# Kernel optimization log

Hardware: AMD Instinct MI355X
Metric: run time of the kernel (lower is better)

## Reference

```python
import jax, jax.numpy as jnp
import numpy as np

N_NODES = 15000
N_EDGES = 40000
N_GRAPHS = 750
D = 64
NODE_DIM = 32
EDGE_DIM = 16
NUM_CONV = 3
S2S_STEPS = 3


def setup_inputs() -> dict:
    key = jax.random.key(0)
    ks = jax.random.split(key, 24)
    s = 0.05
    inp = {
        'x': jax.random.normal(ks[0], (N_NODES, NODE_DIM), jnp.float32),
        'edge_attr': jax.random.uniform(ks[1], (N_EDGES, EDGE_DIM), jnp.float32),
        'edge_index': jax.random.randint(ks[2], (2, N_EDGES), 0, N_NODES),
        'batch': jnp.sort(jax.random.randint(ks[3], (N_NODES,), 0, N_GRAPHS)),
        # input projection
        'in_W': jax.random.normal(ks[4], (NODE_DIM, D)) * s,
        'in_b': jnp.zeros((D,)),
        # edge MLP -> per-edge DxD weights
        'e1_W': jax.random.normal(ks[5], (EDGE_DIM, D)) * s,
        'e1_b': jnp.zeros((D,)),
        'e2_W': jax.random.normal(ks[6], (D, D * D)) * s,
        'e2_b': jnp.zeros((D * D,)),
        'conv_b': jnp.zeros((D,)),
        # GRU (gate order r,z,n like torch)
        'gru_Wih': jax.random.normal(ks[7], (3 * D, D)) * s,
        'gru_Whh': jax.random.normal(ks[8], (3 * D, D)) * s,
        'gru_bih': jnp.zeros((3 * D,)),
        'gru_bhh': jnp.zeros((3 * D,)),
        # Set2Set LSTM (gate order i,f,g,o like torch), input 2D -> hidden D
        'lstm_Wih': jax.random.normal(ks[9], (4 * D, 2 * D)) * s,
        'lstm_Whh': jax.random.normal(ks[10], (4 * D, D)) * s,
        'lstm_bih': jnp.zeros((4 * D,)),
        'lstm_bhh': jnp.zeros((4 * D,)),
        # output MLP
        'out1_W': jax.random.normal(ks[11], (2 * D, 2 * D)) * s,
        'out1_b': jnp.zeros((2 * D,)),
        'out2_W': jax.random.normal(ks[12], (2 * D, 1)) * s,
        'out2_b': jnp.zeros((1,)),
    }
    return inp


def _gru_cell(m, h, Wih, Whh, bih, bhh):
    gi = m @ Wih.T + bih
    gh = h @ Whh.T + bhh
    ir, iz, inn = jnp.split(gi, 3, axis=-1)
    hr, hz, hn = jnp.split(gh, 3, axis=-1)
    r = jax.nn.sigmoid(ir + hr)
    z = jax.nn.sigmoid(iz + hz)
    n = jnp.tanh(inn + r * hn)
    return (1.0 - z) * n + z * h


def _lstm_cell(q, h, c, Wih, Whh, bih, bhh):
    g = q @ Wih.T + bih + h @ Whh.T + bhh
    i, f, gg, o = jnp.split(g, 4, axis=-1)
    c = jax.nn.sigmoid(f) * c + jax.nn.sigmoid(i) * jnp.tanh(gg)
    h = jax.nn.sigmoid(o) * jnp.tanh(c)
    return h, c


def reference(x, edge_attr, edge_index, batch,
              in_W, in_b, e1_W, e1_b, e2_W, e2_b, conv_b,
              gru_Wih, gru_Whh, gru_bih, gru_bhh,
              lstm_Wih, lstm_Whh, lstm_bih, lstm_bhh,
              out1_W, out1_b, out2_W, out2_b):
    src, dst = edge_index[0], edge_index[1]
    out = jax.nn.relu(x @ in_W + in_b)           # [N, D]
    h = out
    # edge-conditioned weights (edge_attr is constant across conv iters)
    W_e = (jax.nn.relu(edge_attr @ e1_W + e1_b) @ e2_W + e2_b).reshape(-1, D, D)  # [E, D, D]
    deg = jnp.maximum(jax.ops.segment_sum(jnp.ones((N_EDGES,), out.dtype), dst, N_NODES), 1.0)
    for _ in range(NUM_CONV):
        msg = jnp.einsum('ed,edf->ef', out[src], W_e)          # per-edge matmul
        agg = jax.ops.segment_sum(msg, dst, N_NODES) / deg[:, None]  # scatter-mean
        m = jax.nn.relu(agg + conv_b)
        h = _gru_cell(m, h, gru_Wih, gru_Whh, gru_bih, gru_bhh)
        out = h
    # Set2Set pooling
    q_star = jnp.zeros((N_GRAPHS, 2 * D), out.dtype)
    hl = jnp.zeros((N_GRAPHS, D), out.dtype)
    cl = jnp.zeros((N_GRAPHS, D), out.dtype)
    for _ in range(S2S_STEPS):
        hl, cl = _lstm_cell(q_star, hl, cl, lstm_Wih, lstm_Whh, lstm_bih, lstm_bhh)
        q = hl
        e = jnp.sum(out * q[batch], axis=-1)                    # [N]
        e = e - jax.ops.segment_max(e, batch, N_GRAPHS)[batch]
        ee = jnp.exp(e)
        a = ee / jax.ops.segment_sum(ee, batch, N_GRAPHS)[batch]
        r = jax.ops.segment_sum(a[:, None] * out, batch, N_GRAPHS)  # [G, D]
        q_star = jnp.concatenate([q, r], axis=-1)
    z = jax.nn.relu(q_star @ out1_W + out1_b) @ out2_W + out2_b
    return z
```

## Files before the change

### kernel.cpp

```cpp
#include <hip/hip_runtime.h>
#include <math.h>

#define N_NODES 15000
#define N_EDGES 40000
#define N_GRAPHS 750
#define N_TILES 938
#define N_TILES_PAD 944

typedef __attribute__((ext_vector_type(8))) short bf16x8;
typedef __attribute__((ext_vector_type(4))) float f32x4;

__device__ __forceinline__ float sigmoidf_(float x) { return 1.f / (1.f + expf(-x)); }

__device__ __forceinline__ unsigned short f2bf(float v) {
    unsigned u = __float_as_uint(v);
    unsigned r = (u + 0x7FFFu + ((u >> 16) & 1u)) >> 16;
    return (unsigned short)r;
}
__device__ __forceinline__ float bf2f(unsigned short b) {
    return __uint_as_float(((unsigned)b) << 16);
}


__global__ void tscan_kernel(const int* __restrict__ tcnt, int* __restrict__ tptr,
                             int* __restrict__ cursor) {
    __shared__ int buf[1024];
    int t = threadIdx.x;
    int v = (t < N_TILES) ? tcnt[t] : 0;
    buf[t] = v;
    __syncthreads();
    for (int ofs = 1; ofs < 1024; ofs <<= 1) {
        int a = (t >= ofs) ? buf[t - ofs] : 0;
        __syncthreads();
        buf[t] += a;
        __syncthreads();
    }
    int excl = buf[t] - v;
    if (t <= N_TILES_PAD) tptr[t] = excl;
    if (t < N_TILES) cursor[t] = excl;
}

__global__ void fillpack_kernel(const int* __restrict__ src, int* __restrict__ cursor,
                                int* __restrict__ edge_list,
                                const float* __restrict__ node_h,
                                unsigned short* __restrict__ Apack) {
    int b = blockIdx.x;
    int tid = threadIdx.x;
    if (b < 157) {
        int e = b * 256 + tid;
        if (e < N_EDGES) {
            int slot = atomicAdd(&cursor[src[e] >> 4], 1);
            edge_list[slot] = e;
        }
    } else {
        int nt = b - 157;
        for (int idx = tid; idx < 1024; idx += 256) {
            int kt = idx >> 9, lane = (idx >> 3) & 63, j = idx & 7;
            int quad = lane >> 4, m = lane & 15;
            int n = nt * 16 + m;
            float v = (n < N_NODES) ? node_h[(size_t)n * 64 + kt * 32 + quad * 8 + j] : 0.f;
            unsigned short hi = f2bf(v);
            Apack[nt * 2048 + kt * 1024 + lane * 8 + j] = hi;
            Apack[nt * 2048 + kt * 1024 + 512 + lane * 8 + j] = f2bf(v - bf2f(hi));
        }
    }
}

__global__ __launch_bounds__(256)
void prep_kernel(const float* __restrict__ x, const float* __restrict__ in_W,
                 const float* __restrict__ in_b, float* __restrict__ node_h,
                 const float* __restrict__ e2b,
                 const float* __restrict__ ea, const float* __restrict__ e1_W,
                 const float* __restrict__ e1_b, float* __restrict__ h1,
                 const float* __restrict__ e2W,
                 unsigned short* __restrict__ Bhi, unsigned short* __restrict__ Blo,
                 const float* __restrict__ lWih, const float* __restrict__ lWhh,
                 const float* __restrict__ gWih, const float* __restrict__ gWhh,
                 float* __restrict__ lWihT, float* __restrict__ lWhhT,
                 unsigned short* __restrict__ gWihP, unsigned short* __restrict__ gWhhP,
                 const int* __restrict__ batch, int* __restrict__ gptr,
                 const int* __restrict__ src, const int* __restrict__ dst,
                 int* __restrict__ tcnt, float* __restrict__ deg) {
    int b = blockIdx.x;
    int tid = threadIdx.x;
    if (b < 938) {
        __shared__ float xs[4][32];
        int n0 = b * 16;
        for (int g2 = 0; g2 < 4; ++g2) {
            int nb = n0 + g2 * 4;
            __syncthreads();
            if (tid < 128) {
                int xi = nb * 32 + tid;
                xs[tid >> 5][tid & 31] = (xi < N_NODES * 32) ? x[xi] : 0.f;
            }
            __syncthreads();
            int nn = tid >> 6, f = tid & 63;
            float s = in_b[f];
            #pragma unroll
            for (int i = 0; i < 32; ++i) s += xs[nn][i] * in_W[i * 64 + f];
            if (nb + nn < N_NODES) node_h[(size_t)(nb + nn) * 64 + f] = fmaxf(s, 0.f);
        }
    } else if (b < 2188) {
        __shared__ float eas[4][16];
        int e0 = (b - 938) * 32;
        for (int g2 = 0; g2 < 8; ++g2) {
            int eb = e0 + g2 * 4;
            __syncthreads();
            if (tid < 64) eas[tid >> 4][tid & 15] = ea[eb * 16 + tid];
            __syncthreads();
            int nn = tid >> 6, f = tid & 63;
            float s = e1_b[f];
            #pragma unroll
            for (int i = 0; i < 16; ++i) s += eas[nn][i] * e1_W[i * 64 + f];
            h1[(size_t)(eb + nn) * 64 + f] = fmaxf(s, 0.f);
        }
    } else if (b < 3244) {
        int idx = (b - 2188) * 256 + tid;
        int j = idx & 7, lane = (idx >> 3) & 63, kt = (idx >> 9) & 1;
        int rem = idx >> 10;
        int ct = rem % 33, ft = rem / 33;
        int d = kt * 32 + ((lane >> 4) << 3) + j;
        int m = lane & 15;
        float v;
        if (ct < 32) {
            int c = ct * 16 + m;
            int kk = c >> 3, fi = c & 7;
            v = e2W[(size_t)kk * 4096 + d * 64 + ft * 8 + fi];
        } else {
            v = (m < 8) ? e2b[d * 64 + ft * 8 + m] : 0.f;
        }
        unsigned short hi = f2bf(v);
        Bhi[idx] = hi;
        Blo[idx] = f2bf(v - bf2f(hi));
    } else if (b < 3436) {
        int idx = (b - 3244) * 256 + tid;
        if (idx < 32768) {
            int i = idx >> 8, r = idx & 255;
            lWihT[i * 256 + r] = lWih[r * 128 + i];
        } else if (idx < 49152) {
            int x2 = idx - 32768; int i = x2 >> 8, r = x2 & 255;
            lWhhT[i * 256 + r] = lWhh[r * 64 + i];
        }
    } else if (b < 3532) {
        int idx = (b - 3436) * 256 + tid;
        if (idx < 12288) {
            int j = idx & 7, lane = (idx >> 3) & 63, kt = (idx >> 9) & 1, ct = idx >> 10;
            int k = kt * 32 + ((lane >> 4) << 3) + j;
            int n = ct * 16 + (lane & 15);
            float v = gWih[n * 64 + k];
            unsigned short hi = f2bf(v);
            gWihP[idx] = hi;
            gWihP[12288 + idx] = f2bf(v - bf2f(hi));
        } else {
            int i2 = idx - 12288;
            int j = i2 & 7, lane = (i2 >> 3) & 63, kt = (i2 >> 9) & 1, ct = i2 >> 10;
            int k = kt * 32 + ((lane >> 4) << 3) + j;
            int n = ct * 16 + (lane & 15);
            float v = gWhh[n * 64 + k];
            unsigned short hi = f2bf(v);
            gWhhP[i2] = hi;
            gWhhP[12288 + i2] = f2bf(v - bf2f(hi));
        }
    } else if (b < 3591) {
        int n = (b - 3532) * 256 + tid;
        if (n < N_NODES) {
            int bb = batch[n];
            int pb = (n == 0) ? -1 : batch[n - 1];
            for (int g = pb + 1; g <= bb; ++g) gptr[g] = n;
            if (n == N_NODES - 1)
                for (int g = bb + 1; g <= N_GRAPHS; ++g) gptr[g] = N_NODES;
        }
    } else {
        int e = (b - 3591) * 256 + tid;
        if (e < N_EDGES) {
            atomicAdd(&tcnt[src[e] >> 4], 1);
            atomicAdd(&deg[dst[e]], 1.f);
        }
    }
}

__global__ __launch_bounds__(256, 4)
void conv_kernel(const unsigned short* __restrict__ Apack, const float* __restrict__ h1,
                 const unsigned short* __restrict__ Bhi, const unsigned short* __restrict__ Blo,
                 const int* __restrict__ tptr, const int* __restrict__ edge_list,
                 const int* __restrict__ src, const int* __restrict__ dst,
                 float* __restrict__ agg) {
    __shared__ float T_lds[16 * 548];
    int bid = blockIdx.x;
    int nt = bid % N_TILES_PAD, ft = bid / N_TILES_PAD;
    int n0 = nt * 16;
    int tid = threadIdx.x;
    int lane = tid & 63, wave = tid >> 6;
    int quad = lane >> 4, m = lane & 15;

    int te0 = tptr[nt], te1 = tptr[nt + 1];
    int fi = tid & 7, slot = tid >> 3;
    int cA = te0 + slot, cB = cA + 32;
    int eA = (cA < te1) ? edge_list[cA] : -1;
    int eB = (cB < te1) ? edge_list[cB] : -1;
    int sA_ = 0, dA_ = 0, sB_ = 0, dB_ = 0;
    float4 pa0 = make_float4(0.f, 0.f, 0.f, 0.f), pa1 = pa0, pb0 = pa0, pb1 = pa0;
    if (eA >= 0) {
        sA_ = src[eA]; dA_ = dst[eA];
        pa0 = *(const float4*)(h1 + (size_t)eA * 64);
        pa1 = *(const float4*)(h1 + (size_t)eA * 64 + 4);
    }
    if (eB >= 0) {
        sB_ = src[eB]; dB_ = dst[eB];
        pb0 = *(const float4*)(h1 + (size_t)eB * 64);
        pb1 = *(const float4*)(h1 + (size_t)eB * 64 + 4);
    }

    const unsigned short* ap = Apack + nt * 2048 + lane * 8;
    bf16x8 ahi[2], alo[2];
    ahi[0] = *(const bf16x8*)(ap);
    alo[0] = *(const bf16x8*)(ap + 512);
    ahi[1] = *(const bf16x8*)(ap + 1024);
    alo[1] = *(const bf16x8*)(ap + 1536);

    size_t base0 = (size_t)(ft * 33 + wave) * 1024 + lane * 8;
    const unsigned short* ph = Bhi + base0;
    const unsigned short* pl = Blo + base0;
    bf16x8 bh0 = *(const bf16x8*)(ph);
    bf16x8 bh1 = *(const bf16x8*)(ph + 512);
    bf16x8 bl0 = *(const bf16x8*)(pl);
    bf16x8 bl1 = *(const bf16x8*)(pl + 512);

    int nct = (wave == 0) ? 9 : 8;
    #pragma unroll 1
    for (int ci = 0; ci < nct; ++ci) {
        bf16x8 ch0 = bh0, ch1 = bh1, cl0 = bl0, cl1 = bl1;
        if (ci + 1 < nct) {
            const unsigned short* nh = ph + (size_t)(ci + 1) * 4096;
            const unsigned short* nl = pl + (size_t)(ci + 1) * 4096;
            bh0 = *(const bf16x8*)(nh);
            bh1 = *(const bf16x8*)(nh + 512);
            bl0 = *(const bf16x8*)(nl);
            bl1 = *(const bf16x8*)(nl + 512);
        }
        f32x4 accA = {0.f, 0.f, 0.f, 0.f};
        f32x4 accB = {0.f, 0.f, 0.f, 0.f};
        accA = __builtin_amdgcn_mfma_f32_16x16x32_bf16(ahi[0], ch0, accA, 0, 0, 0);
        accB = __builtin_amdgcn_mfma_f32_16x16x32_bf16(ahi[1], ch1, accB, 0, 0, 0);
        accA = __builtin_amdgcn_mfma_f32_16x16x32_bf16(alo[0], ch0, accA, 0, 0, 0);
        accB = __builtin_amdgcn_mfma_f32_16x16x32_bf16(alo[1], ch1, accB, 0, 0, 0);
        accA = __builtin_amdgcn_mfma_f32_16x16x32_bf16(ahi[0], cl0, accA, 0, 0, 0);
        accB = __builtin_amdgcn_mfma_f32_16x16x32_bf16(ahi[1], cl1, accB, 0, 0, 0);
        int ct = wave + ci * 4;
        int c = ct * 16 + m;
        int kk = c >> 3, fo = c & 7;
        #pragma unroll
        for (int r = 0; r < 4; ++r)
            T_lds[(quad * 4 + r) * 548 + fo * 68 + kk] = accA[r] + accB[r];
    }
    __syncthreads();

    if (eA >= 0) {
        int nn0 = sA_ - n0;
        int nn1 = (eB >= 0 ? sB_ : sA_) - n0;
        const float* h0p = h1 + (size_t)eA * 64;
        const float* h1p = h1 + (size_t)(eB >= 0 ? eB : eA) * 64;
        const float* T0 = &T_lds[nn0 * 548 + fi * 68];
        const float* T1 = &T_lds[nn1 * 548 + fi * 68];
        float p00 = T0[64], p01 = 0.f, p10 = T1[64], p11 = 0.f;
        {
            float4 ta = *(const float4*)(T0);
            float4 tb = *(const float4*)(T0 + 4);
            float4 tc = *(const float4*)(T1);
            float4 td = *(const float4*)(T1 + 4);
            p00 += pa0.x * ta.x + pa0.y * ta.y + pa0.z * ta.z + pa0.w * ta.w;
            p01 += pa1.x * tb.x + pa1.y * tb.y + pa1.z * tb.z + pa1.w * tb.w;
            p10 += pb0.x * tc.x + pb0.y * tc.y + pb0.z * tc.z + pb0.w * tc.w;
            p11 += pb1.x * td.x + pb1.y * td.y + pb1.z * td.z + pb1.w * td.w;
        }
        #pragma unroll
        for (int k4 = 8; k4 < 64; k4 += 8) {
            float4 ha = *(const float4*)(h0p + k4);
            float4 ta = *(const float4*)(T0 + k4);
            float4 hb = *(const float4*)(h0p + k4 + 4);
            float4 tb = *(const float4*)(T0 + k4 + 4);
            float4 hc = *(const float4*)(h1p + k4);
            float4 tc = *(const float4*)(T1 + k4);
            float4 hd = *(const float4*)(h1p + k4 + 4);
            float4 td = *(const float4*)(T1 + k4 + 4);
            p00 += ha.x * ta.x + ha.y * ta.y + ha.z * ta.z + ha.w * ta.w;
            p01 += hb.x * tb.x + hb.y * tb.y + hb.z * tb.z + hb.w * tb.w;
            p10 += hc.x * tc.x + hc.y * tc.y + hc.z * tc.z + hc.w * tc.w;
            p11 += hd.x * td.x + hd.y * td.y + hd.z * td.z + hd.w * td.w;
        }
        atomicAdd(&agg[(size_t)dA_ * 64 + ft * 8 + fi], p00 + p01);
        if (eB >= 0) atomicAdd(&agg[(size_t)dB_ * 64 + ft * 8 + fi], p10 + p11);
    }
    for (int c = cA + 64; c < te1; c += 64) {
        int c1 = c + 32;
        bool h2 = (c1 < te1);
        int e0 = edge_list[c];
        int e1 = h2 ? edge_list[c1] : e0;
        int nn0 = src[e0] - n0, nn1 = src[e1] - n0;
        const float* h0p = h1 + (size_t)e0 * 64;
        const float* h1p = h1 + (size_t)e1 * 64;
        const float* T0 = &T_lds[nn0 * 548 + fi * 68];
        const float* T1 = &T_lds[nn1 * 548 + fi * 68];
        float p00 = T0[64], p01 = 0.f, p10 = T1[64], p11 = 0.f;
        #pragma unroll
        for (int k4 = 0; k4 < 64; k4 += 8) {
            float4 ha = *(const float4*)(h0p + k4);
            float4 ta = *(const float4*)(T0 + k4);
            float4 hb = *(const float4*)(h0p + k4 + 4);
            float4 tb = *(const float4*)(T0 + k4 + 4);
            float4 hc = *(const float4*)(h1p + k4);
            float4 tc = *(const float4*)(T1 + k4);
            float4 hd = *(const float4*)(h1p + k4 + 4);
            float4 td = *(const float4*)(T1 + k4 + 4);
            p00 += ha.x * ta.x + ha.y * ta.y + ha.z * ta.z + ha.w * ta.w;
            p01 += hb.x * tb.x + hb.y * tb.y + hb.z * tb.z + hb.w * tb.w;
            p10 += hc.x * tc.x + hc.y * tc.y + hc.z * tc.z + hc.w * tc.w;
            p11 += hd.x * td.x + hd.y * td.y + hd.z * td.z + hd.w * td.w;
        }
        atomicAdd(&agg[(size_t)dst[e0] * 64 + ft * 8 + fi], p00 + p01);
        if (h2) atomicAdd(&agg[(size_t)dst[e1] * 64 + ft * 8 + fi], p10 + p11);
    }
}

__global__ __launch_bounds__(256, 4)
void gru_kernel(float* __restrict__ node_h, float* __restrict__ agg,
                const float* __restrict__ deg, const float* __restrict__ conv_b,
                const unsigned short* __restrict__ WihP, const unsigned short* __restrict__ WhhP,
                const float* __restrict__ bih, const float* __restrict__ bhh,
                unsigned short* __restrict__ Apack, int want_pack) {
    __shared__ unsigned short m_bf[2][32][72];
    __shared__ unsigned short h_bf[2][32][72];
    __shared__ float h_s[32][68];
    __shared__ float hn_s[32][68];
    int n0 = blockIdx.x * 32;
    int tid = threadIdx.x;
    int lane = tid & 63, w = tid >> 6;
    int quad = lane >> 4, m16 = lane & 15;

    for (int i = tid; i < 2048; i += 256) {
        int c = i >> 6, f = i & 63;
        int n = n0 + c;
        float mv = 0.f, hv = 0.f;
        if (n < N_NODES) {
            float dg = fmaxf(deg[n], 1.f);
            mv = fmaxf(agg[(size_t)n * 64 + f] / dg + conv_b[f], 0.f);
            agg[(size_t)n * 64 + f] = 0.f;
            hv = node_h[(size_t)n * 64 + f];
        }
        unsigned short mh = f2bf(mv);
        m_bf[0][c][f] = mh; m_bf[1][c][f] = f2bf(mv - bf2f(mh));
        unsigned short hh = f2bf(hv);
        h_bf[0][c][f] = hh; h_bf[1][c][f] = f2bf(hv - bf2f(hh));
        h_s[c][f] = hv;
    }

    bf16x8 Bi[3][2][2], Bh[3][2][2];
    #pragma unroll
    for (int g = 0; g < 3; ++g)
        #pragma unroll
        for (int kt = 0; kt < 2; ++kt) {
            size_t base = ((size_t)((g * 4 + w) * 2 + kt) * 64 + lane) * 8;
            Bi[g][kt][0] = *(const bf16x8*)(WihP + base);
            Bi[g][kt][1] = *(const bf16x8*)(WihP + 12288 + base);
            Bh[g][kt][0] = *(const bf16x8*)(WhhP + base);
            Bh[g][kt][1] = *(const bf16x8*)(WhhP + 12288 + base);
        }
    int f = w * 16 + m16;
    float br_i = bih[f],       br_h = bhh[f];
    float bz_i = bih[64 + f],  bz_h = bhh[64 + f];
    float bn_i = bih[128 + f], bn_h = bhh[128 + f];
    __syncthreads();

    #pragma unroll 1
    for (int mt = 0; mt < 2; ++mt) {
        bf16x8 Am[2][2], Ah[2][2];
        #pragma unroll
        for (int kt = 0; kt < 2; ++kt) {
            Am[kt][0] = *(const bf16x8*)(&m_bf[0][mt * 16 + m16][kt * 32 + quad * 8]);
            Am[kt][1] = *(const bf16x8*)(&m_bf[1][mt * 16 + m16][kt * 32 + quad * 8]);
            Ah[kt][0] = *(const bf16x8*)(&h_bf[0][mt * 16 + m16][kt * 32 + quad * 8]);
            Ah[kt][1] = *(const bf16x8*)(&h_bf[1][mt * 16 + m16][kt * 32 + quad * 8]);
        }
        f32x4 ai[3], ah[3];
        #pragma unroll
        for (int g = 0; g < 3; ++g) { ai[g] = (f32x4){0.f,0.f,0.f,0.f}; ah[g] = (f32x4){0.f,0.f,0.f,0.f}; }
        #pragma unroll
        for (int g = 0; g < 3; ++g)
            #pragma unroll
            for (int kt = 0; kt < 2; ++kt) {
                ai[g] = __builtin_amdgcn_mfma_f32_16x16x32_bf16(Am[kt][0], Bi[g][kt][0], ai[g], 0, 0, 0);
                ai[g] = __builtin_amdgcn_mfma_f32_16x16x32_bf16(Am[kt][0], Bi[g][kt][1], ai[g], 0, 0, 0);
                ai[g] = __builtin_amdgcn_mfma_f32_16x16x32_bf16(Am[kt][1], Bi[g][kt][0], ai[g], 0, 0, 0);
                ah[g] = __builtin_amdgcn_mfma_f32_16x16x32_bf16(Ah[kt][0], Bh[g][kt][0], ah[g], 0, 0, 0);
                ah[g] = __builtin_amdgcn_mfma_f32_16x16x32_bf16(Ah[kt][0], Bh[g][kt][1], ah[g], 0, 0, 0);
                ah[g] = __builtin_amdgcn_mfma_f32_16x16x32_bf16(Ah[kt][1], Bh[g][kt][0], ah[g], 0, 0, 0);
            }
        #pragma unroll
        for (int r = 0; r < 4; ++r) {
            int node = mt * 16 + quad * 4 + r;
            float rr = sigmoidf_(ai[0][r] + br_i + ah[0][r] + br_h);
            float zz = sigmoidf_(ai[1][r] + bz_i + ah[1][r] + bz_h);
            float n2 = tanhf(ai[2][r] + bn_i + rr * (ah[2][r] + bn_h));
            float hnew = (1.f - zz) * n2 + zz * h_s[node][f];
            int n = n0 + node;
            if (n < N_NODES) node_h[(size_t)n * 64 + f] = hnew;
            hn_s[node][f] = hnew;
        }
    }
    if (want_pack) {
        __syncthreads();
        for (int idx = tid; idx < 2048; idx += 256) {
            int tt = idx >> 10, r2 = idx & 1023;
            int kt = r2 >> 9, ln = (r2 >> 3) & 63, j = r2 & 7;
            int q2 = ln >> 4, mm = ln & 15;
            float v = hn_s[tt * 16 + mm][kt * 32 + q2 * 8 + j];
            unsigned short hi = f2bf(v);
            size_t base = (size_t)(blockIdx.x * 2 + tt) * 2048 + kt * 1024 + ln * 8 + j;
            Apack[base] = hi;
            Apack[base + 512] = f2bf(v - bf2f(hi));
        }
    }
}

__global__ __launch_bounds__(256)
void s2s_kernel(const float* __restrict__ node_h, const int* __restrict__ gptr,
                const float* __restrict__ WihT, const float* __restrict__ WhhT,
                const float* __restrict__ bih, const float* __restrict__ bhh,
                const float* __restrict__ o1W, const float* __restrict__ o1b,
                const float* __restrict__ o2W, const float* __restrict__ o2b,
                float* __restrict__ z) {
    int g = blockIdx.x, tid = threadIdx.x;
    int f = tid & 63, q = tid >> 6;
    __shared__ float qs[128], hs[64], qv[64], wts[256], gvs[4][64], racc_s[4][64];
    __shared__ float mred[4], sred[4], ored[2];
    if (q == 0) { qs[f] = 0.f; qs[64 + f] = 0.f; hs[f] = 0.f; }
    float c_t = 0.f;
    int nbeg = gptr[g], nend = gptr[g + 1];
    __syncthreads();
    for (int st = 0; st < 3; ++st) {
        {
            int row = q * 64 + f;
            float s = bih[row] + bhh[row];
            #pragma unroll 8
            for (int i = 0; i < 128; ++i) s += qs[i] * WihT[i * 256 + row];
            #pragma unroll 8
            for (int i = 0; i < 64; ++i) s += hs[i] * WhhT[i * 256 + row];
            gvs[q][f] = s;
        }
        __syncthreads();
        if (q == 0) {
            float c = sigmoidf_(gvs[1][f]) * c_t + sigmoidf_(gvs[0][f]) * tanhf(gvs[2][f]);
            float hn = sigmoidf_(gvs[3][f]) * tanhf(c);
            c_t = c;
            hs[f] = hn; qv[f] = hn;
        }
        __syncthreads();
        float rm = -INFINITY, rs = 0.f, raccl = 0.f;
        for (int base = nbeg; base < nend; base += 256) {
            int n = base + tid;
            float e = -INFINITY;
            if (n < nend) {
                float s = 0.f;
                #pragma unroll 8
                for (int ff = 0; ff < 64; ++ff) s += node_h[(size_t)n * 64 + ff] * qv[ff];
                e = s;
            }
            float cm = e;
            #pragma unroll
            for (int o = 32; o > 0; o >>= 1) cm = fmaxf(cm, __shfl_down(cm, o));
            if ((tid & 63) == 0) mred[q] = cm;
            __syncthreads();
            float bm = fmaxf(fmaxf(mred[0], mred[1]), fmaxf(mred[2], mred[3]));
            float nm = fmaxf(rm, bm);
            float scale = (rm == -INFINITY) ? 0.f : expf(rm - nm);
            float wv = (n < nend) ? expf(e - nm) : 0.f;
            wts[tid] = wv;
            float cs = wv;
            #pragma unroll
            for (int o = 32; o > 0; o >>= 1) cs += __shfl_down(cs, o);
            if ((tid & 63) == 0) sred[q] = cs;
            __syncthreads();
            float bs = (sred[0] + sred[1]) + (sred[2] + sred[3]);
            float na = raccl * scale;
            int cnt2 = min(256, nend - base);
            int l0 = q * 64, l1 = min(l0 + 64, cnt2);
            for (int l = l0; l < l1; ++l) na += wts[l] * node_h[(size_t)(base + l) * 64 + f];
            raccl = na;
            rs = rs * scale + bs;
            rm = nm;
            __syncthreads();
        }
        racc_s[q][f] = raccl;
        __syncthreads();
        if (q == 0) {
            float r = (nend > nbeg)
                    ? ((racc_s[0][f] + racc_s[1][f]) + (racc_s[2][f] + racc_s[3][f])) / rs
                    : 0.f;
            qs[f] = qv[f];
            qs[64 + f] = r;
        }
        __syncthreads();
    }
    if (tid < 128) {
        float sA = o1b[tid];
        #pragma unroll 8
        for (int i = 0; i < 128; ++i) sA += qs[i] * o1W[i * 128 + tid];
        float red = fmaxf(sA, 0.f) * o2W[tid];
        #pragma unroll
        for (int o = 32; o > 0; o >>= 1) red += __shfl_down(red, o);
        if ((tid & 63) == 0) ored[tid >> 6] = red;
    }
    __syncthreads();
    if (tid == 0) z[g] = ored[0] + ored[1] + o2b[0];
}

extern "C" void kernel_launch(void* const* d_in, const int* in_sizes, int n_in,
                              void* d_out, int out_size, void* d_ws, size_t ws_size,
                              hipStream_t stream) {
    const float* x         = (const float*)d_in[0];
    const float* edge_attr = (const float*)d_in[1];
    const int*   ei        = (const int*)d_in[2];
    const int*   batch     = (const int*)d_in[3];
    const float* in_W      = (const float*)d_in[4];
    const float* in_b      = (const float*)d_in[5];
    const float* e1_W      = (const float*)d_in[6];
    const float* e1_b      = (const float*)d_in[7];
    const float* e2_W      = (const float*)d_in[8];
    const float* e2_b      = (const float*)d_in[9];
    const float* conv_b    = (const float*)d_in[10];
    const float* gWih      = (const float*)d_in[11];
    const float* gWhh      = (const float*)d_in[12];
    const float* gbih      = (const float*)d_in[13];
    const float* gbhh      = (const float*)d_in[14];
    const float* lWih      = (const float*)d_in[15];
    const float* lWhh      = (const float*)d_in[16];
    const float* lbih      = (const float*)d_in[17];
    const float* lbhh      = (const float*)d_in[18];
    const float* o1W       = (const float*)d_in[19];
    const float* o1b       = (const float*)d_in[20];
    const float* o2W       = (const float*)d_in[21];
    const float* o2b       = (const float*)d_in[22];
    const int* src = ei;
    const int* dst = ei + N_EDGES;
    float* z = (float*)d_out;

    char* ws = (char*)d_ws;
    size_t off = 0;
    auto alloc = [&](size_t bytes) {
        void* p = ws + off;
        off = (off + bytes + 255) & ~(size_t)255;
        return p;
    };
    float* node_h   = (float*)alloc((size_t)N_NODES * 64 * 4);
    float* agg      = (float*)alloc((size_t)N_NODES * 64 * 4);
    float* h1       = (float*)alloc((size_t)N_EDGES * 64 * 4);
    unsigned short* Bhi = (unsigned short*)alloc((size_t)270336 * 2);
    unsigned short* Blo = (unsigned short*)alloc((size_t)270336 * 2);
    unsigned short* Apack = (unsigned short*)alloc((size_t)N_TILES_PAD * 2048 * 2);
    float* lWihT    = (float*)alloc(128 * 256 * 4);
    float* lWhhT    = (float*)alloc(64 * 256 * 4);
    unsigned short* gWihP = (unsigned short*)alloc(24576 * 2);
    unsigned short* gWhhP = (unsigned short*)alloc(24576 * 2);
    float* deg      = (float*)alloc(N_NODES * 4);
    int*   tcnt     = (int*)alloc((N_TILES + 2) * 4);
    int*   tcursor  = (int*)alloc((N_TILES + 2) * 4);
    int*   tptr     = (int*)alloc((N_TILES_PAD + 2) * 4);
    int*   edge_list= (int*)alloc(N_EDGES * 4);
    int*   gptr     = (int*)alloc((N_GRAPHS + 1) * 4);

    size_t degpad = ((size_t)N_NODES * 4 + 255) & ~(size_t)255;
    hipMemsetAsync(deg, 0, degpad + (N_TILES + 2) * 4, stream);
    hipMemsetAsync(agg, 0, (size_t)N_NODES * 64 * 4, stream);

    prep_kernel<<<3748, 256, 0, stream>>>(x, in_W, in_b, node_h, e2_b,
                                          edge_attr, e1_W, e1_b, h1,
                                          e2_W, Bhi, Blo,
                                          lWih, lWhh, gWih, gWhh,
                                          lWihT, lWhhT, gWihP, gWhhP,
                                          batch, gptr, src, dst, tcnt, deg);
    tscan_kernel<<<1, 1024, 0, stream>>>(tcnt, tptr, tcursor);
    fillpack_kernel<<<157 + N_TILES_PAD, 256, 0, stream>>>(src, tcursor, edge_list,
                                                           node_h, Apack);

    for (int it = 0; it < 3; ++it) {
        conv_kernel<<<N_TILES_PAD * 8, 256, 0, stream>>>(Apack, h1, Bhi, Blo,
                                                         tptr, edge_list, src, dst, agg);
        gru_kernel<<<469, 256, 0, stream>>>(node_h, agg, deg, conv_b,
                                            gWihP, gWhhP, gbih, gbhh,
                                            Apack, (it < 2) ? 1 : 0);
    }
    s2s_kernel<<<N_GRAPHS, 256, 0, stream>>>(node_h, gptr, lWihT, lWhhT, lbih, lbhh,
                                             o1W, o1b, o2W, o2b, z);
}
```

Baseline: 430.3 us.

## Split conv output features into 16 groups of 4 per block

```diff
diff --git a/kernel.cpp b/kernel.cpp
--- a/kernel.cpp
+++ b/kernel.cpp
@@ -114,26 +114,28 @@
             for (int i = 0; i < 16; ++i) s += eas[nn][i] * e1_W[i * 64 + f];
             h1[(size_t)(eb + nn) * 64 + f] = fmaxf(s, 0.f);
         }
-    } else if (b < 3244) {
+    } else if (b < 3276) {
         int idx = (b - 2188) * 256 + tid;
         int j = idx & 7, lane = (idx >> 3) & 63, kt = (idx >> 9) & 1;
         int rem = idx >> 10;
-        int ct = rem % 33, ft = rem / 33;
+        int ct = rem % 17, fq = rem / 17;
         int d = kt * 32 + ((lane >> 4) << 3) + j;
         int m = lane & 15;
+        int c = ct * 16 + m;
         float v;
-        if (ct < 32) {
-            int c = ct * 16 + m;
-            int kk = c >> 3, fi = c & 7;
-            v = e2W[(size_t)kk * 4096 + d * 64 + ft * 8 + fi];
+        if (c < 256) {
+            int kk = c >> 2, fi = c & 3;
+            v = e2W[(size_t)kk * 4096 + d * 64 + fq * 4 + fi];
+        } else if (c < 260) {
+            v = e2b[d * 64 + fq * 4 + (c & 3)];
         } else {
-            v = (m < 8) ? e2b[d * 64 + ft * 8 + m] : 0.f;
+            v = 0.f;
         }
         unsigned short hi = f2bf(v);
         Bhi[idx] = hi;
         Blo[idx] = f2bf(v - bf2f(hi));
-    } else if (b < 3436) {
-        int idx = (b - 3244) * 256 + tid;
+    } else if (b < 3468) {
+        int idx = (b - 3276) * 256 + tid;
         if (idx < 32768) {
             int i = idx >> 8, r = idx & 255;
             lWihT[i * 256 + r] = lWih[r * 128 + i];
@@ -141,8 +143,8 @@
             int x2 = idx - 32768; int i = x2 >> 8, r = x2 & 255;
             lWhhT[i * 256 + r] = lWhh[r * 64 + i];
         }
-    } else if (b < 3532) {
-        int idx = (b - 3436) * 256 + tid;
+    } else if (b < 3564) {
+        int idx = (b - 3468) * 256 + tid;
         if (idx < 12288) {
             int j = idx & 7, lane = (idx >> 3) & 63, kt = (idx >> 9) & 1, ct = idx >> 10;
             int k = kt * 32 + ((lane >> 4) << 3) + j;
@@ -161,8 +163,8 @@
             gWhhP[i2] = hi;
             gWhhP[12288 + i2] = f2bf(v - bf2f(hi));
         }
-    } else if (b < 3591) {
-        int n = (b - 3532) * 256 + tid;
+    } else if (b < 3623) {
+        int n = (b - 3564) * 256 + tid;
         if (n < N_NODES) {
             int bb = batch[n];
             int pb = (n == 0) ? -1 : batch[n - 1];
@@ -171,7 +173,7 @@
                 for (int g = bb + 1; g <= N_GRAPHS; ++g) gptr[g] = N_NODES;
         }
     } else {
-        int e = (b - 3591) * 256 + tid;
+        int e = (b - 3623) * 256 + tid;
         if (e < N_EDGES) {
             atomicAdd(&tcnt[src[e] >> 4], 1);
             atomicAdd(&deg[dst[e]], 1.f);
@@ -179,36 +181,30 @@
     }
 }
 
-__global__ __launch_bounds__(256, 4)
+__global__ __launch_bounds__(256, 6)
 void conv_kernel(const unsigned short* __restrict__ Apack, const float* __restrict__ h1,
                  const unsigned short* __restrict__ Bhi, const unsigned short* __restrict__ Blo,
                  const int* __restrict__ tptr, const int* __restrict__ edge_list,
                  const int* __restrict__ src, const int* __restrict__ dst,
                  float* __restrict__ agg) {
-    __shared__ float T_lds[16 * 548];
+    __shared__ float T_lds[16 * 276];
     int bid = blockIdx.x;
-    int nt = bid % N_TILES_PAD, ft = bid / N_TILES_PAD;
+    int nt = bid % N_TILES_PAD, fq = bid / N_TILES_PAD;
     int n0 = nt * 16;
     int tid = threadIdx.x;
     int lane = tid & 63, wave = tid >> 6;
     int quad = lane >> 4, m = lane & 15;
 
     int te0 = tptr[nt], te1 = tptr[nt + 1];
-    int fi = tid & 7, slot = tid >> 3;
-    int cA = te0 + slot, cB = cA + 32;
+    int fi = tid & 3, slot = tid >> 2;
+    int cA = te0 + slot;
     int eA = (cA < te1) ? edge_list[cA] : -1;
-    int eB = (cB < te1) ? edge_list[cB] : -1;
-    int sA_ = 0, dA_ = 0, sB_ = 0, dB_ = 0;
-    float4 pa0 = make_float4(0.f, 0.f, 0.f, 0.f), pa1 = pa0, pb0 = pa0, pb1 = pa0;
+    int sA_ = 0, dA_ = 0;
+    float4 pa0 = make_float4(0.f, 0.f, 0.f, 0.f), pa1 = pa0;
     if (eA >= 0) {
         sA_ = src[eA]; dA_ = dst[eA];
         pa0 = *(const float4*)(h1 + (size_t)eA * 64);
         pa1 = *(const float4*)(h1 + (size_t)eA * 64 + 4);
-    }
-    if (eB >= 0) {
-        sB_ = src[eB]; dB_ = dst[eB];
-        pb0 = *(const float4*)(h1 + (size_t)eB * 64);
-        pb1 = *(const float4*)(h1 + (size_t)eB * 64 + 4);
     }
 
     const unsigned short* ap = Apack + nt * 2048 + lane * 8;
@@ -218,7 +214,7 @@
     ahi[1] = *(const bf16x8*)(ap + 1024);
     alo[1] = *(const bf16x8*)(ap + 1536);
 
-    size_t base0 = (size_t)(ft * 33 + wave) * 1024 + lane * 8;
+    size_t base0 = (size_t)(fq * 17 + wave) * 1024 + lane * 8;
     const unsigned short* ph = Bhi + base0;
     const unsigned short* pl = Blo + base0;
     bf16x8 bh0 = *(const bf16x8*)(ph);
@@ -226,7 +222,7 @@
     bf16x8 bl0 = *(const bf16x8*)(pl);
     bf16x8 bl1 = *(const bf16x8*)(pl + 512);
 
-    int nct = (wave == 0) ? 9 : 8;
+    int nct = (wave == 0) ? 5 : 4;
     #pragma unroll 1
     for (int ci = 0; ci < nct; ++ci) {
         bf16x8 ch0 = bh0, ch1 = bh1, cl0 = bl0, cl1 = bl1;
@@ -248,30 +244,23 @@
         accB = __builtin_amdgcn_mfma_f32_16x16x32_bf16(ahi[1], cl1, accB, 0, 0, 0);
         int ct = wave + ci * 4;
         int c = ct * 16 + m;
-        int kk = c >> 3, fo = c & 7;
+        int kk = c >> 2, fo = c & 3;
         #pragma unroll
         for (int r = 0; r < 4; ++r)
-            T_lds[(quad * 4 + r) * 548 + fo * 68 + kk] = accA[r] + accB[r];
+            T_lds[(quad * 4 + r) * 276 + fo * 68 + kk] = accA[r] + accB[r];
     }
     __syncthreads();
 
     if (eA >= 0) {
         int nn0 = sA_ - n0;
-        int nn1 = (eB >= 0 ? sB_ : sA_) - n0;
         const float* h0p = h1 + (size_t)eA * 64;
-        const float* h1p = h1 + (size_t)(eB >= 0 ? eB : eA) * 64;
-        const float* T0 = &T_lds[nn0 * 548 + fi * 68];
-        const float* T1 = &T_lds[nn1 * 548 + fi * 68];
-        float p00 = T0[64], p01 = 0.f, p10 = T1[64], p11 = 0.f;
+        const float* T0 = &T_lds[nn0 * 276 + fi * 68];
+        float p00 = T0[64], p01 = 0.f;
         {
             float4 ta = *(const float4*)(T0);
             float4 tb = *(const float4*)(T0 + 4);
-            float4 tc = *(const float4*)(T1);
-            float4 td = *(const float4*)(T1 + 4);
             p00 += pa0.x * ta.x + pa0.y * ta.y + pa0.z * ta.z + pa0.w * ta.w;
             p01 += pa1.x * tb.x + pa1.y * tb.y + pa1.z * tb.z + pa1.w * tb.w;
-            p10 += pb0.x * tc.x + pb0.y * tc.y + pb0.z * tc.z + pb0.w * tc.w;
-            p11 += pb1.x * td.x + pb1.y * td.y + pb1.z * td.z + pb1.w * td.w;
         }
         #pragma unroll
         for (int k4 = 8; k4 < 64; k4 += 8) {
@@ -279,46 +268,27 @@
             float4 ta = *(const float4*)(T0 + k4);
             float4 hb = *(const float4*)(h0p + k4 + 4);
             float4 tb = *(const float4*)(T0 + k4 + 4);
-            float4 hc = *(const float4*)(h1p + k4);
-            float4 tc = *(const float4*)(T1 + k4);
-            float4 hd = *(const float4*)(h1p + k4 + 4);
-            float4 td = *(const float4*)(T1 + k4 + 4);
             p00 += ha.x * ta.x + ha.y * ta.y + ha.z * ta.z + ha.w * ta.w;
             p01 += hb.x * tb.x + hb.y * tb.y + hb.z * tb.z + hb.w * tb.w;
-            p10 += hc.x * tc.x + hc.y * tc.y + hc.z * tc.z + hc.w * tc.w;
-            p11 += hd.x * td.x + hd.y * td.y + hd.z * td.z + hd.w * td.w;
-        }
-        atomicAdd(&agg[(size_t)dA_ * 64 + ft * 8 + fi], p00 + p01);
-        if (eB >= 0) atomicAdd(&agg[(size_t)dB_ * 64 + ft * 8 + fi], p10 + p11);
+        }
+        atomicAdd(&agg[(size_t)dA_ * 64 + fq * 4 + fi], p00 + p01);
     }
     for (int c = cA + 64; c < te1; c += 64) {
-        int c1 = c + 32;
-        bool h2 = (c1 < te1);
         int e0 = edge_list[c];
-        int e1 = h2 ? edge_list[c1] : e0;
-        int nn0 = src[e0] - n0, nn1 = src[e1] - n0;
+        int nn0 = src[e0] - n0;
         const float* h0p = h1 + (size_t)e0 * 64;
-        const float* h1p = h1 + (size_t)e1 * 64;
-        const float* T0 = &T_lds[nn0 * 548 + fi * 68];
-        const float* T1 = &T_lds[nn1 * 548 + fi * 68];
-        float p00 = T0[64], p01 = 0.f, p10 = T1[64], p11 = 0.f;
+        const float* T0 = &T_lds[nn0 * 276 + fi * 68];
+        float p00 = T0[64], p01 = 0.f;
         #pragma unroll
         for (int k4 = 0; k4 < 64; k4 += 8) {
             float4 ha = *(const float4*)(h0p + k4);
             float4 ta = *(const float4*)(T0 + k4);
             float4 hb = *(const float4*)(h0p + k4 + 4);
             float4 tb = *(const float4*)(T0 + k4 + 4);
-            float4 hc = *(const float4*)(h1p + k4);
-            float4 tc = *(const float4*)(T1 + k4);
-            float4 hd = *(const float4*)(h1p + k4 + 4);
-            float4 td = *(const float4*)(T1 + k4 + 4);
             p00 += ha.x * ta.x + ha.y * ta.y + ha.z * ta.z + ha.w * ta.w;
             p01 += hb.x * tb.x + hb.y * tb.y + hb.z * tb.z + hb.w * tb.w;
-            p10 += hc.x * tc.x + hc.y * tc.y + hc.z * tc.z + hc.w * tc.w;
-            p11 += hd.x * td.x + hd.y * td.y + hd.z * td.z + hd.w * td.w;
-        }
-        atomicAdd(&agg[(size_t)dst[e0] * 64 + ft * 8 + fi], p00 + p01);
-        if (h2) atomicAdd(&agg[(size_t)dst[e1] * 64 + ft * 8 + fi], p10 + p11);
+        }
+        atomicAdd(&agg[(size_t)dst[e0] * 64 + fq * 4 + fi], p00 + p01);
     }
 }
 
@@ -554,8 +524,8 @@
     float* node_h   = (float*)alloc((size_t)N_NODES * 64 * 4);
     float* agg      = (float*)alloc((size_t)N_NODES * 64 * 4);
     float* h1       = (float*)alloc((size_t)N_EDGES * 64 * 4);
-    unsigned short* Bhi = (unsigned short*)alloc((size_t)270336 * 2);
-    unsigned short* Blo = (unsigned short*)alloc((size_t)270336 * 2);
+    unsigned short* Bhi = (unsigned short*)alloc((size_t)278528 * 2);
+    unsigned short* Blo = (unsigned short*)alloc((size_t)278528 * 2);
     unsigned short* Apack = (unsigned short*)alloc((size_t)N_TILES_PAD * 2048 * 2);
     float* lWihT    = (float*)alloc(128 * 256 * 4);
     float* lWhhT    = (float*)alloc(64 * 256 * 4);
@@ -572,7 +542,7 @@
     hipMemsetAsync(deg, 0, degpad + (N_TILES + 2) * 4, stream);
     hipMemsetAsync(agg, 0, (size_t)N_NODES * 64 * 4, stream);
 
-    prep_kernel<<<3748, 256, 0, stream>>>(x, in_W, in_b, node_h, e2_b,
+    prep_kernel<<<3780, 256, 0, stream>>>(x, in_W, in_b, node_h, e2_b,
                                           edge_attr, e1_W, e1_b, h1,
                                           e2_W, Bhi, Blo,
                                           lWih, lWhh, gWih, gWhh,
@@ -583,8 +553,8 @@
                                                            node_h, Apack);
 
     for (int it = 0; it < 3; ++it) {
-        conv_kernel<<<N_TILES_PAD * 8, 256, 0, stream>>>(Apack, h1, Bhi, Blo,
-                                                         tptr, edge_list, src, dst, agg);
+        conv_kernel<<<N_TILES_PAD * 16, 256, 0, stream>>>(Apack, h1, Bhi, Blo,
+                                                          tptr, edge_list, src, dst, agg);
         gru_kernel<<<469, 256, 0, stream>>>(node_h, agg, deg, conv_b,
                                             gWihP, gWhhP, gbih, gbhh,
                                             Apack, (it < 2) ? 1 : 0);
```

Result: slower. 439.2 us (+2.1%).
